# Optimization experiments

Measured on AMD Instinct MI355X. Metric: run time of the kernel, lower is better.

The kernel has to match this reference:

```python
import jax, jax.numpy as jnp
import numpy as np

# BQQ block dims: Y_sign (p,j,k,m,l), Z_sign (p,j,k,l,n); in=k*n=4096, out=j*m=4096
P, J, K, M, L, N = 2, 32, 32, 128, 16, 128
ACT_BITS = 8  # activation quantization bits


def setup_inputs() -> dict:
    key = jax.random.key(0)
    ks = jax.random.split(key, 7)
    x = jax.random.normal(ks[0], (1, 512, K * N), dtype=jnp.float32)
    # sign matrices in {-1,+1}
    Y_sign = jnp.where(jax.random.normal(ks[1], (P, J, K, M, L)) >= 0, 1.0, -1.0).astype(jnp.float32)
    Z_sign = jnp.where(jax.random.normal(ks[2], (P, J, K, L, N)) >= 0, 1.0, -1.0).astype(jnp.float32)
    # per-block positive scales (abs-mean in the original, so strictly > 0)
    Y_scale = jax.random.uniform(ks[3], (P, J, K, 1, 1), minval=0.01, maxval=0.1, dtype=jnp.float32)
    Z_scale = jax.random.uniform(ks[4], (P, J, K, 1, 1), minval=0.01, maxval=0.1, dtype=jnp.float32)
    A = jax.random.normal(ks[5], (P, J, K, 4), dtype=jnp.float32) * 0.1
    bias = jax.random.normal(ks[6], (J * M,), dtype=jnp.float32) * 0.1
    return {"input": x, "Y_sign": Y_sign, "Z_sign": Z_sign,
            "Y_scale": Y_scale, "Z_scale": Z_scale, "A": A, "bias": bias}


def reference(input, Y_sign, Z_sign, Y_scale, Z_scale, A, bias):
    # --- activation quantization (act_bits = 8, simple round, no STE) ---
    qmax = float(2 ** (ACT_BITS - 1) - 1)  # 127
    x_max = jnp.max(input)
    x_min = jnp.min(input)
    act_scale = jnp.maximum((x_max - x_min) / (2.0 * qmax), 1e-8)
    X = jnp.clip(jnp.round(input / act_scale), -qmax, qmax) * act_scale

    # --- dequantize sign * scale ---
    Y_q = Y_sign * Y_scale  # (p,j,k,m,l)
    Z_q = Z_sign * Z_scale  # (p,j,k,l,n)

    orig_shape = X.shape[:-1]
    X_kn = X.reshape(-1, K, N)  # (B,k,n)

    # chained block einsums
    T = jnp.einsum('bkn,pjkln->bpjkl', X_kn, Z_q)          # (B,p,j,k,l)
    core = jnp.einsum('pjkml,bpjkl->bpjkm', Y_q, T)        # (B,p,j,k,m)

    # quant_bias=True correction terms: A[...,0..3] = (a,b,c,d)
    out1 = jnp.einsum('bpjkm,pjk->bjm', core, A[..., 0])

    Y_sum = Y_q.sum(axis=-1)                               # (p,j,k,m)
    B_coef = jnp.einsum('pjk,pjkm->jkm', A[..., 1], Y_sum)
    Sx = X_kn.sum(axis=-1)                                 # (B,k)
    out2 = jnp.einsum('bk,jkm->bjm', Sx, B_coef)

    Zs = Z_q.sum(axis=-2)                                  # (p,j,k,n)
    Tz = jnp.einsum('bkn,pjkn->bpjk', X_kn, Zs)
    out3 = jnp.einsum('bpjk,pjk->bj', Tz, A[..., 2])

    D_coef = A[..., 3].sum(axis=0)                         # (j,k)
    out4 = jnp.einsum('bk,jk->bj', Sx, D_coef)

    out_bjm = out1 + out2 + (out3 + out4)[:, :, None]      # (B,j,m)
    out_2d = out_bjm.reshape(-1, J * M) + bias
    return out_2d.reshape(*orig_shape, J * M)
```

## Files before the change

### kernel.cpp

```cpp
#include <hip/hip_runtime.h>
#include <hip/hip_bf16.h>

typedef __attribute__((ext_vector_type(4))) float f32x4;
typedef __attribute__((ext_vector_type(8))) short bf16x8;
typedef __attribute__((ext_vector_type(4))) unsigned int u32x4;

#define GLOBAL_AS __attribute__((address_space(1)))
#define LDS_AS __attribute__((address_space(3)))

static __device__ __forceinline__ unsigned short f2bf(float f) {
  __hip_bfloat16 h = __float2bfloat16(f);
  return __builtin_bit_cast(unsigned short, h);
}
static __device__ __forceinline__ float bf2f(unsigned short u) {
  unsigned int v = ((unsigned int)u) << 16;
  return __builtin_bit_cast(float, v);
}
static __device__ __forceinline__ void load_lds16(const void* g, void* l) {
  __builtin_amdgcn_global_load_lds((GLOBAL_AS void*)g, (LDS_AS void*)l, 16, 0, 0);
}

__global__ __launch_bounds__(256) void k_minmax_part(const float* __restrict__ x,
                                                     float* __restrict__ part) {
  int tid = blockIdx.x * 256 + threadIdx.x;
  const float4* xv = (const float4*)x;
  float mn = 3.4e38f, mx = -3.4e38f;
#pragma unroll
  for (int rep = 0; rep < 8; ++rep) {
    float4 v = xv[tid + rep * 65536];
    mn = fminf(mn, fminf(fminf(v.x, v.y), fminf(v.z, v.w)));
    mx = fmaxf(mx, fmaxf(fmaxf(v.x, v.y), fmaxf(v.z, v.w)));
  }
#pragma unroll
  for (int o = 32; o > 0; o >>= 1) {
    mn = fminf(mn, __shfl_down(mn, o));
    mx = fmaxf(mx, __shfl_down(mx, o));
  }
  __shared__ float smn[4], smx[4];
  int lane = threadIdx.x & 63, w = threadIdx.x >> 6;
  if (lane == 0) { smn[w] = mn; smx[w] = mx; }
  __syncthreads();
  if (threadIdx.x == 0) {
    mn = fminf(fminf(smn[0], smn[1]), fminf(smn[2], smn[3]));
    mx = fmaxf(fmaxf(smx[0], smx[1]), fmaxf(smx[2], smx[3]));
    part[2 * blockIdx.x] = mn;
    part[2 * blockIdx.x + 1] = mx;
  }
}

__global__ __launch_bounds__(256) void k_fused(const float* __restrict__ x,
                                               const float* __restrict__ part,
                                               const float* __restrict__ Ysg,
                                               const float* __restrict__ Zsg,
                                               const float* __restrict__ Ysc,
                                               const float* __restrict__ Zsc,
                                               const float* __restrict__ Acoef,
                                               float* __restrict__ scl,
                                               unsigned short* __restrict__ xq,
                                               unsigned short* __restrict__ W) {
  const int t = threadIdx.x;
  if (blockIdx.x < 1024) {
    const int jk = blockIdx.x;
    __shared__ unsigned short Yb[2 * 128 * 24];
    __shared__ unsigned short Zb[128 * 36];
    __shared__ float B1p[2][128];
    __shared__ float C1[128];
    float cf0[2], cf2[2], cf4[2];
    float Dv;
    {
      float ys0 = Ysc[jk], zs0 = Zsc[jk], ys1 = Ysc[1024 + jk], zs1 = Zsc[1024 + jk];
      const float* A0p = Acoef + (size_t)jk * 4;
      const float* A1p = Acoef + (size_t)(1024 + jk) * 4;
      cf0[0] = A0p[0] * ys0 * zs0; cf0[1] = A1p[0] * ys1 * zs1;
      cf2[0] = A0p[1] * ys0;       cf2[1] = A1p[1] * ys1;
      cf4[0] = A0p[2] * zs0;       cf4[1] = A1p[2] * zs1;
      Dv = A0p[3] + A1p[3];
    }
#pragma unroll
    for (int rep = 0; rep < 4; ++rep) {
      int q = rep * 256 + t;
      int l0 = (q & 3) * 4, m = (q >> 2) & 127, p = q >> 9;
      float4 v = *(const float4*)(Ysg + (size_t)(p * 1024 + jk) * 2048 + m * 16 + l0);
      float s4 = v.x + v.y + v.z + v.w;
      s4 += __shfl_xor(s4, 1);
      s4 += __shfl_xor(s4, 2);
      if ((t & 3) == 0) B1p[p][m] = s4;
      float c0 = cf0[p];
      ushort4 o = make_ushort4(f2bf(c0 * v.x), f2bf(c0 * v.y), f2bf(c0 * v.z), f2bf(c0 * v.w));
      *(ushort4*)&Yb[(p * 128 + m) * 24 + l0] = o;
    }
#pragma unroll
    for (int rep = 0; rep < 4; ++rep) {
      int q = rep * 256 + t;
      int n0 = (q & 31) * 4, l = (q >> 5) & 15, p = q >> 9;
      float4 v = *(const float4*)(Zsg + (size_t)(p * 1024 + jk) * 2048 + l * 128 + n0);
      int pl = p * 16 + l;
      Zb[(n0 + 0) * 36 + pl] = f2bf(v.x);
      Zb[(n0 + 1) * 36 + pl] = f2bf(v.y);
      Zb[(n0 + 2) * 36 + pl] = f2bf(v.z);
      Zb[(n0 + 3) * 36 + pl] = f2bf(v.w);
    }
    __syncthreads();
    if (t < 128) {
      float s0 = 0.f, s1 = 0.f;
#pragma unroll
      for (int l = 0; l < 16; ++l) {
        s0 += bf2f(Zb[t * 36 + l]);
        s1 += bf2f(Zb[t * 36 + 16 + l]);
      }
      C1[t] = cf4[0] * s0 + cf4[1] * s1;
    }
    __syncthreads();
    const int lane = t & 63, wid = t >> 6;
    const int wm = wid >> 1, wn = wid & 1;
    const int grp = lane >> 4;
    bf16x8 af[4], bfr[4];
#pragma unroll
    for (int fm = 0; fm < 4; ++fm) {
      int m = wm * 64 + fm * 16 + (lane & 15);
      af[fm] = *(const bf16x8*)((const char*)Yb + ((grp >> 1) * 128 + m) * 48 + (grp & 1) * 16);
    }
#pragma unroll
    for (int fn = 0; fn < 4; ++fn) {
      int n = wn * 64 + fn * 16 + (lane & 15);
      const char* zp = (const char*)Zb + n * 72 + grp * 16;
      uint2 z0 = *(const uint2*)zp;
      uint2 z1 = *(const uint2*)(zp + 8);
      u32x4 zw; zw[0] = z0.x; zw[1] = z0.y; zw[2] = z1.x; zw[3] = z1.y;
      bfr[fn] = __builtin_bit_cast(bf16x8, zw);
    }
    f32x4 acc[4][4];
#pragma unroll
    for (int fm = 0; fm < 4; ++fm)
#pragma unroll
      for (int fn = 0; fn < 4; ++fn)
        acc[fm][fn] = __builtin_amdgcn_mfma_f32_16x16x32_bf16(af[fm], bfr[fn], (f32x4)(0.f), 0, 0, 0);
    const int j = jk >> 5, k = jk & 31;
    float c1v[4];
#pragma unroll
    for (int fn = 0; fn < 4; ++fn) c1v[fn] = C1[wn * 64 + fn * 16 + (lane & 15)];
#pragma unroll
    for (int fm = 0; fm < 4; ++fm) {
#pragma unroll
      for (int i = 0; i < 4; ++i) {
        int row = wm * 64 + fm * 16 + (grp)*4 + i;
        float b1v = cf2[0] * B1p[0][row] + cf2[1] * B1p[1][row] + Dv;
        size_t rowoff = (size_t)(j * 128 + row) * 4096 + (size_t)(k * 128);
#pragma unroll
        for (int fn = 0; fn < 4; ++fn) {
          int col = wn * 64 + fn * 16 + (lane & 15);
          W[rowoff + col] = f2bf(acc[fm][fn][i] + b1v + c1v[fn]);
        }
      }
    }
  } else {
    const int qb = blockIdx.x - 1024;
    float2 v2 = ((const float2*)part)[t];
    float mn = v2.x, mx = v2.y;
#pragma unroll
    for (int o = 32; o > 0; o >>= 1) {
      mn = fminf(mn, __shfl_down(mn, o));
      mx = fmaxf(mx, __shfl_down(mx, o));
    }
    __shared__ float smn2[4], smx2[4], ssc[1];
    int lane = t & 63, w = t >> 6;
    if (lane == 0) { smn2[w] = mn; smx2[w] = mx; }
    __syncthreads();
    if (t == 0) {
      mn = fminf(fminf(smn2[0], smn2[1]), fminf(smn2[2], smn2[3]));
      mx = fmaxf(fmaxf(smx2[0], smx2[1]), fmaxf(smx2[2], smx2[3]));
      ssc[0] = fmaxf((mx - mn) / 254.0f, 1e-8f);
      if (qb == 0) scl[0] = ssc[0];
    }
    __syncthreads();
    const float s = ssc[0];
    int i = qb * 256 + t;
    float4 v = ((const float4*)x)[i];
    float a = fminf(fmaxf(rintf(v.x / s), -127.f), 127.f);
    float b = fminf(fmaxf(rintf(v.y / s), -127.f), 127.f);
    float c = fminf(fmaxf(rintf(v.z / s), -127.f), 127.f);
    float d = fminf(fmaxf(rintf(v.w / s), -127.f), 127.f);
    ((ushort4*)xq)[i] = make_ushort4(f2bf(a), f2bf(b), f2bf(c), f2bf(d));
  }
}

__global__ __launch_bounds__(512) void k_gemm(const unsigned short* __restrict__ Xq,
                                              const unsigned short* __restrict__ W,
                                              float* __restrict__ out,
                                              unsigned short* __restrict__ P) {
  __shared__ unsigned short Al[3][256 * 64];
  __shared__ unsigned short Bl[3][128 * 64];
  const int t = threadIdx.x, lane = t & 63, wid = t >> 6;
  const int wg = (blockIdx.x & 7) * 32 + (blockIdx.x >> 3);
  const int bn = wg >> 3;
  const int sk = (wg >> 1) & 3;
  const int bm = wg & 1;
  const int wm = wid >> 1, wn = wid & 1;
  const int kbase = sk * 1024;
  f32x4 acc[4][4];
#pragma unroll
  for (int a = 0; a < 4; ++a)
#pragma unroll
    for (int b = 0; b < 4; ++b) acc[a][b] = (f32x4)(0.f);

  const int lr = lane >> 3;
  const int lcb = (lane & 7) * 16;

  auto STAGE = [&](int buf, int kt) {
    const int k0 = kbase + kt * 64;
#pragma unroll
    for (int c = 0; c < 4; ++c) {
      int chunk = wid * 4 + c;
      int r = chunk * 8 + lr;
      int colb = lcb ^ ((r & 7) << 4);
      load_lds16(Xq + ((size_t)(bm * 256 + r) << 12) + k0 + (colb >> 1), &Al[buf][chunk * 512]);
    }
#pragma unroll
    for (int c = 0; c < 2; ++c) {
      int chunk = wid * 2 + c;
      int r = chunk * 8 + lr;
      int colb = lcb ^ ((r & 7) << 4);
      load_lds16(W + ((size_t)(bn * 128 + r) << 12) + k0 + (colb >> 1), &Bl[buf][chunk * 512]);
    }
  };

  auto COMPUTE = [&](int buf) {
#pragma unroll
    for (int ks = 0; ks < 2; ++ks) {
      bf16x8 af[4], bfr[4];
#pragma unroll
      for (int fm = 0; fm < 4; ++fm) {
        int r = wm * 64 + fm * 16 + (lane & 15);
        int colb = (ks * 64 + ((lane >> 4) * 16)) ^ ((r & 7) << 4);
        af[fm] = *(const bf16x8*)((const char*)&Al[buf][0] + r * 128 + colb);
      }
#pragma unroll
      for (int fn = 0; fn < 4; ++fn) {
        int r = wn * 64 + fn * 16 + (lane & 15);
        int colb = (ks * 64 + ((lane >> 4) * 16)) ^ ((r & 7) << 4);
        bfr[fn] = *(const bf16x8*)((const char*)&Bl[buf][0] + r * 128 + colb);
      }
#pragma unroll
      for (int fm = 0; fm < 4; ++fm)
#pragma unroll
        for (int fn = 0; fn < 4; ++fn)
          acc[fm][fn] = __builtin_amdgcn_mfma_f32_16x16x32_bf16(af[fm], bfr[fn], acc[fm][fn], 0, 0, 0);
    }
  };

  STAGE(0, 0);
  STAGE(1, 1);
  int b0 = 2;
  for (int it = 0; it < 16; ++it) {
    STAGE(b0, (it + 2) & 15);
    __builtin_amdgcn_sched_barrier(0);
    asm volatile("s_waitcnt vmcnt(12)" ::: "memory");
    __builtin_amdgcn_sched_barrier(0);
    __builtin_amdgcn_s_barrier();
    __builtin_amdgcn_sched_barrier(0);
    int cb = b0 + 1;
    if (cb >= 3) cb -= 3;
    COMPUTE(cb);
    __builtin_amdgcn_sched_barrier(0);
    __builtin_amdgcn_s_barrier();
    b0 = cb;
  }

  if (sk == 0) {
#pragma unroll
    for (int fn = 0; fn < 4; ++fn) {
      int col = bn * 128 + wn * 64 + fn * 16 + (lane & 15);
#pragma unroll
      for (int fm = 0; fm < 4; ++fm) {
#pragma unroll
        for (int i = 0; i < 4; ++i) {
          int row = bm * 256 + wm * 64 + fm * 16 + (lane >> 4) * 4 + i;
          out[(size_t)row * 4096 + col] = acc[fm][fn][i];
        }
      }
    }
  } else {
    unsigned short* Pk = P + (size_t)(sk - 1) * 2097152;
#pragma unroll
    for (int fn = 0; fn < 4; ++fn) {
      int col = bn * 128 + wn * 64 + fn * 16 + (lane & 15);
#pragma unroll
      for (int fm = 0; fm < 4; ++fm) {
#pragma unroll
        for (int i = 0; i < 4; ++i) {
          int row = bm * 256 + wm * 64 + fm * 16 + (lane >> 4) * 4 + i;
          Pk[(size_t)row * 4096 + col] = f2bf(acc[fm][fn][i]);
        }
      }
    }
  }
}

__global__ __launch_bounds__(256) void k_epi(float* __restrict__ out,
                                             const unsigned short* __restrict__ P,
                                             const float* __restrict__ scl,
                                             const float* __restrict__ bias) {
  int i4 = blockIdx.x * 256 + threadIdx.x;
  const float s = scl[0];
  float4 r = ((const float4*)out)[i4];
  float4 bv = ((const float4*)bias)[i4 & 1023];
  float sx = r.x, sy = r.y, sz = r.z, sw = r.w;
#pragma unroll
  for (int k = 0; k < 3; ++k) {
    ushort4 p = ((const ushort4*)(P + (size_t)k * 2097152))[i4];
    sx += bf2f(p.x); sy += bf2f(p.y); sz += bf2f(p.z); sw += bf2f(p.w);
  }
  ((float4*)out)[i4] = make_float4(sx * s + bv.x, sy * s + bv.y, sz * s + bv.z, sw * s + bv.w);
}

__global__ __launch_bounds__(512) void k_gemm_fb(const unsigned short* __restrict__ Xq,
                                                 const unsigned short* __restrict__ W,
                                                 const float* __restrict__ scl,
                                                 const float* __restrict__ bias,
                                                 float* __restrict__ out) {
  __shared__ unsigned short Al[4][128 * 64];
  __shared__ unsigned short Bl[4][64 * 64];
  const int t = threadIdx.x, lane = t & 63, wid = t >> 6;
  const int wg = (blockIdx.x & 7) * 32 + (blockIdx.x >> 3);
  const int bm = wg & 3;
  const int bn = wg >> 2;
  const int wm = wid >> 1, wn = wid & 1;
  f32x4 acc[2][2];
#pragma unroll
  for (int a = 0; a < 2; ++a)
#pragma unroll
    for (int b = 0; b < 2; ++b) acc[a][b] = (f32x4)(0.f);
  const int lr = lane >> 3;
  const int lcb = (lane & 7) * 16;
  auto STAGE = [&](int buf, int kt) {
    const int k0 = kt * 64;
#pragma unroll
    for (int c = 0; c < 2; ++c) {
      int chunk = wid * 2 + c;
      int r = chunk * 8 + lr;
      int colb = lcb ^ ((r & 7) << 4);
      load_lds16(Xq + ((size_t)(bm * 128 + r) << 12) + k0 + (colb >> 1), &Al[buf][chunk * 512]);
    }
    {
      int r = wid * 8 + lr;
      int colb = lcb ^ ((r & 7) << 4);
      load_lds16(W + ((size_t)(bn * 64 + r) << 12) + k0 + (colb >> 1), &Bl[buf][wid * 512]);
    }
  };
  auto COMPUTE = [&](int buf) {
#pragma unroll
    for (int ks = 0; ks < 2; ++ks) {
      bf16x8 af[2], bfr[2];
#pragma unroll
      for (int fm = 0; fm < 2; ++fm) {
        int r = wm * 32 + fm * 16 + (lane & 15);
        int colb = (ks * 64 + ((lane >> 4) * 16)) ^ ((r & 7) << 4);
        af[fm] = *(const bf16x8*)((const char*)&Al[buf][0] + r * 128 + colb);
      }
#pragma unroll
      for (int fn = 0; fn < 2; ++fn) {
        int r = wn * 32 + fn * 16 + (lane & 15);
        int colb = (ks * 64 + ((lane >> 4) * 16)) ^ ((r & 7) << 4);
        bfr[fn] = *(const bf16x8*)((const char*)&Bl[buf][0] + r * 128 + colb);
      }
#pragma unroll
      for (int fm = 0; fm < 2; ++fm)
#pragma unroll
        for (int fn = 0; fn < 2; ++fn)
          acc[fm][fn] = __builtin_amdgcn_mfma_f32_16x16x32_bf16(af[fm], bfr[fn], acc[fm][fn], 0, 0, 0);
    }
  };
  STAGE(0, 0); STAGE(1, 1); STAGE(2, 2);
  for (int t64 = 0; t64 < 64; ++t64) {
    STAGE((t64 + 3) & 3, (t64 + 3) & 63);
    __builtin_amdgcn_sched_barrier(0);
    asm volatile("s_waitcnt vmcnt(9)" ::: "memory");
    __builtin_amdgcn_sched_barrier(0);
    __builtin_amdgcn_s_barrier();
    __builtin_amdgcn_sched_barrier(0);
    COMPUTE(t64 & 3);
    __builtin_amdgcn_sched_barrier(0);
    __builtin_amdgcn_s_barrier();
  }
  const float s = scl[0];
#pragma unroll
  for (int fn = 0; fn < 2; ++fn) {
    int col = bn * 64 + wn * 32 + fn * 16 + (lane & 15);
    float bv = bias[col];
#pragma unroll
    for (int fm = 0; fm < 2; ++fm) {
#pragma unroll
      for (int i = 0; i < 4; ++i) {
        int row = bm * 128 + wm * 32 + fm * 16 + (lane >> 4) * 4 + i;
        out[(size_t)row * 4096 + col] = acc[fm][fn][i] * s + bv;
      }
    }
  }
}

extern "C" void kernel_launch(void* const* d_in, const int* in_sizes, int n_in,
                              void* d_out, int out_size, void* d_ws, size_t ws_size,
                              hipStream_t stream) {
  const float* x    = (const float*)d_in[0];
  const float* Ysg  = (const float*)d_in[1];
  const float* Zsg  = (const float*)d_in[2];
  const float* Ysc  = (const float*)d_in[3];
  const float* Zsc  = (const float*)d_in[4];
  const float* A    = (const float*)d_in[5];
  const float* bias = (const float*)d_in[6];
  float* out = (float*)d_out;

  char* ws = (char*)d_ws;
  float* scl  = (float*)ws;
  float* part = (float*)(ws + 256);
  unsigned short* Xq = (unsigned short*)(ws + 65536);
  unsigned short* W  = (unsigned short*)(ws + 65536 + (size_t)4194304);
  unsigned short* P  = (unsigned short*)(ws + 65536 + (size_t)4194304 + (size_t)33554432);

  k_minmax_part<<<dim3(256), dim3(256), 0, stream>>>(x, part);
  k_fused<<<dim3(3072), dim3(256), 0, stream>>>(x, part, Ysg, Zsg, Ysc, Zsc, A, scl, Xq, W);
  if (ws_size >= (size_t)65536 + 4194304 + 33554432 + 12582912) {
    k_gemm<<<dim3(256), dim3(512), 0, stream>>>(Xq, W, out, P);
    k_epi<<<dim3(2048), dim3(256), 0, stream>>>(out, P, scl, bias);
  } else {
    k_gemm_fb<<<dim3(256), dim3(512), 0, stream>>>(Xq, W, scl, bias, out);
  }
}
```

Baseline: 56.93 us.

## Use smaller 128x128 GEMM tiles with 8-way split-K and fragment-ordered partials

Replaces the 256x128-tile, 4-way split-K, triple-buffered GEMM with a 128x128 tile, 8-way split-K kernel of 256 threads and 1024 blocks, using a simple single-buffer load/sync/compute loop. Partial sums are written in MFMA fragment order as packed ushort4 so the stores are contiguous, and the epilogue reduces seven bf16 partials and maps them back to row/col. The aim is more blocks to fill the CUs, with fewer LDS bytes per block so several blocks can share a CU. The cost is losing the software pipeline, roughly double the partial-sum traffic, and a larger workspace requirement.

```diff
diff --git a/kernel.cpp b/kernel.cpp
--- a/kernel.cpp
+++ b/kernel.cpp
@@ -184,19 +184,19 @@
   }
 }
 
-__global__ __launch_bounds__(512) void k_gemm(const unsigned short* __restrict__ Xq,
+__global__ __launch_bounds__(256) void k_gemm(const unsigned short* __restrict__ Xq,
                                               const unsigned short* __restrict__ W,
                                               float* __restrict__ out,
                                               unsigned short* __restrict__ P) {
-  __shared__ unsigned short Al[3][256 * 64];
-  __shared__ unsigned short Bl[3][128 * 64];
+  __shared__ unsigned short Al[128 * 64];
+  __shared__ unsigned short Bl[128 * 64];
   const int t = threadIdx.x, lane = t & 63, wid = t >> 6;
-  const int wg = (blockIdx.x & 7) * 32 + (blockIdx.x >> 3);
-  const int bn = wg >> 3;
-  const int sk = (wg >> 1) & 3;
-  const int bm = wg & 1;
+  const int wg = (blockIdx.x & 7) * 128 + (blockIdx.x >> 3);
+  const int sk = wg >> 7;
+  const int bm = (wg >> 5) & 3;
+  const int bn = wg & 31;
   const int wm = wid >> 1, wn = wid & 1;
-  const int kbase = sk * 1024;
+  const int kbase = sk * 512;
   f32x4 acc[4][4];
 #pragma unroll
   for (int a = 0; a < 4; ++a)
@@ -206,25 +206,23 @@
   const int lr = lane >> 3;
   const int lcb = (lane & 7) * 16;
 
-  auto STAGE = [&](int buf, int kt) {
+  for (int kt = 0; kt < 8; ++kt) {
     const int k0 = kbase + kt * 64;
 #pragma unroll
     for (int c = 0; c < 4; ++c) {
       int chunk = wid * 4 + c;
       int r = chunk * 8 + lr;
       int colb = lcb ^ ((r & 7) << 4);
-      load_lds16(Xq + ((size_t)(bm * 256 + r) << 12) + k0 + (colb >> 1), &Al[buf][chunk * 512]);
-    }
-#pragma unroll
-    for (int c = 0; c < 2; ++c) {
-      int chunk = wid * 2 + c;
+      load_lds16(Xq + ((size_t)(bm * 128 + r) << 12) + k0 + (colb >> 1), &Al[chunk * 512]);
+    }
+#pragma unroll
+    for (int c = 0; c < 4; ++c) {
+      int chunk = wid * 4 + c;
       int r = chunk * 8 + lr;
       int colb = lcb ^ ((r & 7) << 4);
-      load_lds16(W + ((size_t)(bn * 128 + r) << 12) + k0 + (colb >> 1), &Bl[buf][chunk * 512]);
-    }
-  };
-
-  auto COMPUTE = [&](int buf) {
+      load_lds16(W + ((size_t)(bn * 128 + r) << 12) + k0 + (colb >> 1), &Bl[chunk * 512]);
+    }
+    __syncthreads();
 #pragma unroll
     for (int ks = 0; ks < 2; ++ks) {
       bf16x8 af[4], bfr[4];
@@ -232,13 +230,13 @@
       for (int fm = 0; fm < 4; ++fm) {
         int r = wm * 64 + fm * 16 + (lane & 15);
         int colb = (ks * 64 + ((lane >> 4) * 16)) ^ ((r & 7) << 4);
-        af[fm] = *(const bf16x8*)((const char*)&Al[buf][0] + r * 128 + colb);
+        af[fm] = *(const bf16x8*)((const char*)Al + r * 128 + colb);
       }
 #pragma unroll
       for (int fn = 0; fn < 4; ++fn) {
         int r = wn * 64 + fn * 16 + (lane & 15);
         int colb = (ks * 64 + ((lane >> 4) * 16)) ^ ((r & 7) << 4);
-        bfr[fn] = *(const bf16x8*)((const char*)&Bl[buf][0] + r * 128 + colb);
+        bfr[fn] = *(const bf16x8*)((const char*)Bl + r * 128 + colb);
       }
 #pragma unroll
       for (int fm = 0; fm < 4; ++fm)
@@ -246,24 +244,7 @@
         for (int fn = 0; fn < 4; ++fn)
           acc[fm][fn] = __builtin_amdgcn_mfma_f32_16x16x32_bf16(af[fm], bfr[fn], acc[fm][fn], 0, 0, 0);
     }
-  };
-
-  STAGE(0, 0);
-  STAGE(1, 1);
-  int b0 = 2;
-  for (int it = 0; it < 16; ++it) {
-    STAGE(b0, (it + 2) & 15);
-    __builtin_amdgcn_sched_barrier(0);
-    asm volatile("s_waitcnt vmcnt(12)" ::: "memory");
-    __builtin_amdgcn_sched_barrier(0);
-    __builtin_amdgcn_s_barrier();
-    __builtin_amdgcn_sched_barrier(0);
-    int cb = b0 + 1;
-    if (cb >= 3) cb -= 3;
-    COMPUTE(cb);
-    __builtin_amdgcn_sched_barrier(0);
-    __builtin_amdgcn_s_barrier();
-    b0 = cb;
+    __syncthreads();
   }
 
   if (sk == 0) {
@@ -274,23 +255,22 @@
       for (int fm = 0; fm < 4; ++fm) {
 #pragma unroll
         for (int i = 0; i < 4; ++i) {
-          int row = bm * 256 + wm * 64 + fm * 16 + (lane >> 4) * 4 + i;
+          int row = bm * 128 + wm * 64 + fm * 16 + (lane >> 4) * 4 + i;
           out[(size_t)row * 4096 + col] = acc[fm][fn][i];
         }
       }
     }
   } else {
     unsigned short* Pk = P + (size_t)(sk - 1) * 2097152;
-#pragma unroll
-    for (int fn = 0; fn < 4; ++fn) {
-      int col = bn * 128 + wn * 64 + fn * 16 + (lane & 15);
-#pragma unroll
-      for (int fm = 0; fm < 4; ++fm) {
-#pragma unroll
-        for (int i = 0; i < 4; ++i) {
-          int row = bm * 256 + wm * 64 + fm * 16 + (lane >> 4) * 4 + i;
-          Pk[(size_t)row * 4096 + col] = f2bf(acc[fm][fn][i]);
-        }
+    const int blkL = bm * 32 + bn;
+#pragma unroll
+    for (int fm = 0; fm < 4; ++fm) {
+#pragma unroll
+      for (int fn = 0; fn < 4; ++fn) {
+        int idx = (((blkL * 4 + wid) * 16 + fm * 4 + fn) * 64) + lane;
+        ushort4 o = make_ushort4(f2bf(acc[fm][fn][0]), f2bf(acc[fm][fn][1]),
+                                 f2bf(acc[fm][fn][2]), f2bf(acc[fm][fn][3]));
+        ((ushort4*)Pk)[idx] = o;
       }
     }
   }
@@ -300,17 +280,28 @@
                                              const unsigned short* __restrict__ P,
                                              const float* __restrict__ scl,
                                              const float* __restrict__ bias) {
-  int i4 = blockIdx.x * 256 + threadIdx.x;
+  int g = blockIdx.x * 256 + threadIdx.x;
+  const int lane = g & 63;
+  const int ff = (g >> 6) & 15;
+  const int fn = ff & 3, fm = ff >> 2;
+  const int wave = (g >> 10) & 3;
+  const int blk = g >> 12;
+  const int bm = blk >> 5, bn = blk & 31;
+  const int wm = wave >> 1, wn = wave & 1;
+  const int row0 = bm * 128 + wm * 64 + fm * 16 + ((lane >> 4) << 2);
+  const int col = bn * 128 + wn * 64 + fn * 16 + (lane & 15);
   const float s = scl[0];
-  float4 r = ((const float4*)out)[i4];
-  float4 bv = ((const float4*)bias)[i4 & 1023];
-  float sx = r.x, sy = r.y, sz = r.z, sw = r.w;
-#pragma unroll
-  for (int k = 0; k < 3; ++k) {
-    ushort4 p = ((const ushort4*)(P + (size_t)k * 2097152))[i4];
-    sx += bf2f(p.x); sy += bf2f(p.y); sz += bf2f(p.z); sw += bf2f(p.w);
-  }
-  ((float4*)out)[i4] = make_float4(sx * s + bv.x, sy * s + bv.y, sz * s + bv.z, sw * s + bv.w);
+  const float bv = bias[col];
+  float sum[4];
+#pragma unroll
+  for (int i = 0; i < 4; ++i) sum[i] = out[(size_t)(row0 + i) * 4096 + col];
+#pragma unroll
+  for (int k = 0; k < 7; ++k) {
+    ushort4 p = ((const ushort4*)(P + (size_t)k * 2097152))[g];
+    sum[0] += bf2f(p.x); sum[1] += bf2f(p.y); sum[2] += bf2f(p.z); sum[3] += bf2f(p.w);
+  }
+#pragma unroll
+  for (int i = 0; i < 4; ++i) out[(size_t)(row0 + i) * 4096 + col] = sum[i] * s + bv;
 }
 
 __global__ __launch_bounds__(512) void k_gemm_fb(const unsigned short* __restrict__ Xq,
@@ -419,8 +410,8 @@
 
   k_minmax_part<<<dim3(256), dim3(256), 0, stream>>>(x, part);
   k_fused<<<dim3(3072), dim3(256), 0, stream>>>(x, part, Ysg, Zsg, Ysc, Zsc, A, scl, Xq, W);
-  if (ws_size >= (size_t)65536 + 4194304 + 33554432 + 12582912) {
-    k_gemm<<<dim3(256), dim3(512), 0, stream>>>(Xq, W, out, P);
+  if (ws_size >= (size_t)65536 + 4194304 + 33554432 + 29360128) {
+    k_gemm<<<dim3(1024), dim3(256), 0, stream>>>(Xq, W, out, P);
     k_epi<<<dim3(2048), dim3(256), 0, stream>>>(out, P, scl, bias);
   } else {
     k_gemm_fb<<<dim3(256), dim3(512), 0, stream>>>(Xq, W, scl, bias, out);
```

New measurement: 61.32 us. 1.08x slower.
